# Performance work log

Measured on AMD Instinct MI355X. Metric: run time of the kernel, lower is better.

The kernel has to match this reference:

```python
import jax, jax.numpy as jnp
import numpy as np

NUM_HEADS = 12
LOCAL_WINDOW = 7


def setup_inputs() -> dict:
    key = jax.random.key(0)
    k1, k2, k3 = jax.random.split(key, 3)
    B, N, C = 2, 2048, 768
    x = jax.random.normal(k1, (B, N, C), dtype=jnp.float32)
    w_qkv = jax.random.normal(k2, (3 * C, C), dtype=jnp.float32) * (C ** -0.5)
    w_proj = jax.random.normal(k3, (C, C), dtype=jnp.float32) * (C ** -0.5)
    b_proj = jnp.zeros((C,), dtype=jnp.float32)
    return {"x": x, "w_qkv": w_qkv, "w_proj": w_proj, "b_proj": b_proj}


def reference(x, w_qkv, w_proj, b_proj):
    B, N, C = x.shape
    H = NUM_HEADS
    Dh = C // H
    scale = Dh ** -0.5
    # local-window additive mask: 0 within |i-j|<=w, -inf outside (vectorized)
    idx = jnp.arange(N)
    local_mask = jnp.where(
        jnp.abs(idx[:, None] - idx[None, :]) <= LOCAL_WINDOW, 0.0, -jnp.inf
    ).astype(x.dtype)
    qkv = x @ w_qkv.T
    qkv = qkv.reshape(B, N, 3, H, Dh).transpose(2, 0, 3, 1, 4)
    q, k, v = qkv[0], qkv[1], qkv[2]
    attn = jnp.einsum("bhnd,bhmd->bhnm", q, k) * scale
    attn = attn + local_mask[None, None, :, :]
    attn = jax.nn.softmax(attn, axis=-1)
    out = jnp.einsum("bhnm,bhmd->bhnd", attn, v)
    out = out.transpose(0, 2, 1, 3).reshape(B, N, C)
    return out @ w_proj.T + b_proj
```

## Files before the change

kernel.cpp:

```cpp
#include <hip/hip_runtime.h>
#include <hip/hip_bf16.h>

typedef __bf16 bf16;
typedef bf16 bf16x4 __attribute__((ext_vector_type(4)));
typedef bf16 bf16x8 __attribute__((ext_vector_type(8)));
typedef float floatx4 __attribute__((ext_vector_type(4)));

#define GLOBAL_AS __attribute__((address_space(1)))
#define LDS_AS __attribute__((address_space(3)))

__global__ __launch_bounds__(256)
void cvt3_f32_bf16(const float* __restrict__ s0, const float* __restrict__ s1,
                   const float* __restrict__ s2, bf16* __restrict__ d0,
                   bf16* __restrict__ d1, bf16* __restrict__ d2,
                   int n0, int n1, int n2)
{
    int t = blockIdx.x * blockDim.x + threadIdx.x;
    const float* s; bf16* d; int i;
    if (t < n0)                { s = s0; d = d0; i = t; }
    else if (t < n0 + n1)      { s = s1; d = d1; i = t - n0; }
    else if (t < n0 + n1 + n2) { s = s2; d = d2; i = t - n0 - n1; }
    else return;
    float4 v = ((const float4*)s)[i];
    bf16x4 o = { (bf16)v.x, (bf16)v.y, (bf16)v.z, (bf16)v.w };
    ((bf16x4*)d)[i] = o;
}

template<typename CT, bool AF32, bool WF32, int TM, int M, int N, int K,
         int LDA, int LDC>
__global__ __launch_bounds__(256, 2)
void gemm_bt(const void* __restrict__ Av, const void* __restrict__ Wv,
             CT* __restrict__ C, const float* __restrict__ bias)
{
    constexpr int MI = TM / 32;
    __shared__ __align__(16) bf16 As[TM * 32];
    __shared__ __align__(16) bf16 Bs[128 * 32];

    const int tid  = threadIdx.x;
    const int lane = tid & 63;
    const int wave = tid >> 6;
    const int row0 = blockIdx.x * TM;
    const int col0 = blockIdx.y * 128;

    const int wm = (wave & 1) * (TM / 2);
    const int wn = (wave >> 1) * 64;

    floatx4 acc[MI][4] = {};

    const int fr = lane & 15;
    const int fk = (lane >> 4) * 8;

    const int lr = lane >> 2;
    const int lk = (lane & 3) * 8;

    for (int k0 = 0; k0 < K; k0 += 32) {
        if (AF32) {
            constexpr int NV = TM * 4;
            #pragma unroll
            for (int c = 0; c < NV / 256; ++c) {
                const int idx = tid + c * 256;
                const int r   = idx >> 2;
                const int cb  = (idx & 3) * 8;
                const float4* g = (const float4*)((const float*)Av
                                   + (size_t)(row0 + r) * LDA + k0 + cb);
                float4 g0 = g[0], g1 = g[1];
                bf16x8 va;
                va[0]=(bf16)g0.x; va[1]=(bf16)g0.y; va[2]=(bf16)g0.z; va[3]=(bf16)g0.w;
                va[4]=(bf16)g1.x; va[5]=(bf16)g1.y; va[6]=(bf16)g1.z; va[7]=(bf16)g1.w;
                *(bf16x8*)(As + r * 32 + cb) = va;
            }
        } else {
            constexpr int CAW = TM / 64;
            #pragma unroll
            for (int c = 0; c < CAW; ++c) {
                const int chunk = wave * CAW + c;
                const int r = chunk * 16 + lr;
                const bf16* gA = (const bf16*)Av + (size_t)(row0 + r) * LDA + k0 + lk;
                __builtin_amdgcn_global_load_lds((const GLOBAL_AS void*)gA,
                                                 (LDS_AS void*)(As + chunk * 512),
                                                 16, 0, 0);
            }
        }
        if (WF32) {
            #pragma unroll
            for (int c = 0; c < 2; ++c) {
                const int idx = tid + c * 256;
                const int r   = idx >> 2;
                const int cb  = (idx & 3) * 8;
                const float4* g = (const float4*)((const float*)Wv
                                   + (size_t)(col0 + r) * K + k0 + cb);
                float4 g0 = g[0], g1 = g[1];
                bf16x8 vw;
                vw[0]=(bf16)g0.x; vw[1]=(bf16)g0.y; vw[2]=(bf16)g0.z; vw[3]=(bf16)g0.w;
                vw[4]=(bf16)g1.x; vw[5]=(bf16)g1.y; vw[6]=(bf16)g1.z; vw[7]=(bf16)g1.w;
                *(bf16x8*)(Bs + r * 32 + cb) = vw;
            }
        } else {
            #pragma unroll
            for (int c = 0; c < 2; ++c) {
                const int chunk = wave * 2 + c;
                const int r = chunk * 16 + lr;
                const bf16* gB = (const bf16*)Wv + (size_t)(col0 + r) * K + k0 + lk;
                __builtin_amdgcn_global_load_lds((const GLOBAL_AS void*)gB,
                                                 (LDS_AS void*)(Bs + chunk * 512),
                                                 16, 0, 0);
            }
        }
        __syncthreads();

        bf16x8 af[MI], bfr[4];
        #pragma unroll
        for (int i = 0; i < MI; ++i)
            af[i]  = *(const bf16x8*)(As + (wm + i * 16 + fr) * 32 + fk);
        #pragma unroll
        for (int j = 0; j < 4; ++j)
            bfr[j] = *(const bf16x8*)(Bs + (wn + j * 16 + fr) * 32 + fk);
        #pragma unroll
        for (int i = 0; i < MI; ++i)
            #pragma unroll
            for (int j = 0; j < 4; ++j)
                acc[i][j] = __builtin_amdgcn_mfma_f32_16x16x32_bf16(
                    af[i], bfr[j], acc[i][j], 0, 0, 0);

        __syncthreads();
    }

    const int fc  = lane & 15;
    const int fr4 = (lane >> 4) * 4;
    #pragma unroll
    for (int i = 0; i < MI; ++i) {
        #pragma unroll
        for (int j = 0; j < 4; ++j) {
            const int col = col0 + wn + j * 16 + fc;
            const float b = bias ? bias[col] : 0.0f;
            #pragma unroll
            for (int r = 0; r < 4; ++r) {
                const int row = row0 + wm + i * 16 + fr4 + r;
                C[(size_t)row * LDC + col] = (CT)(acc[i][j][r] + b);
            }
        }
    }
}

__global__ __launch_bounds__(256)
void attn_tile(const bf16* __restrict__ qkv, bf16* __restrict__ aout)
{
    __shared__ __align__(16) bf16 Ks[4][32][72];
    __shared__ __align__(16) bf16 Vt[4][64][40];
    __shared__ __align__(16) bf16 Ps[4][16][40];

    const int w    = threadIdx.x >> 6;
    const int lane = threadIdx.x & 63;
    const int c    = lane & 15;
    const int q    = lane >> 4;
    const int wid  = blockIdx.x * 4 + w;
    const int it   = wid & 127;
    const int bh   = wid >> 7;
    const int h    = bh % 12;
    const int b    = bh / 12;
    const int I0   = it * 16;
    const int bbase = b * 2048;
    const int j0   = I0 - 7;

    #pragma unroll
    for (int itr = 0; itr < 4; ++itr) {
        int idx = itr * 64 + lane;
        int row = idx >> 3;
        int dc  = (idx & 7) * 8;
        int jc  = j0 + row; jc = jc < 0 ? 0 : (jc > 2047 ? 2047 : jc);
        const bf16* base = qkv + (size_t)(bbase + jc) * 2304 + h * 64 + dc;
        bf16x8 kv = *(const bf16x8*)(base + 768);
        bf16x8 vv = *(const bf16x8*)(base + 1536);
        *(bf16x8*)(&Ks[w][row][dc]) = kv;
        #pragma unroll
        for (int e = 0; e < 8; ++e) Vt[w][dc + e][row] = vv[e];
    }

    const bf16* qrow = qkv + (size_t)(bbase + I0 + c) * 2304 + h * 64;
    bf16x8 aq0 = *(const bf16x8*)(qrow + q * 8);
    bf16x8 aq1 = *(const bf16x8*)(qrow + 32 + q * 8);

    __syncthreads();

    floatx4 st[2] = {};
    #pragma unroll
    for (int t = 0; t < 2; ++t) {
        bf16x8 k0 = *(const bf16x8*)(&Ks[w][t * 16 + c][q * 8]);
        bf16x8 k1 = *(const bf16x8*)(&Ks[w][t * 16 + c][32 + q * 8]);
        st[t] = __builtin_amdgcn_mfma_f32_16x16x32_bf16(aq0, k0, st[t], 0, 0, 0);
        st[t] = __builtin_amdgcn_mfma_f32_16x16x32_bf16(aq1, k1, st[t], 0, 0, 0);
    }

    float s[2][4];
    #pragma unroll
    for (int t = 0; t < 2; ++t)
        #pragma unroll
        for (int r = 0; r < 4; ++r) {
            int il = q * 4 + r;
            int jl = t * 16 + c;
            int ja = j0 + jl;
            bool valid = (jl >= il) && (jl <= il + 14) && (ja >= 0) && (ja < 2048);
            s[t][r] = valid ? st[t][r] * 0.125f : -1e30f;
        }

    float l[4], p[2][4];
    #pragma unroll
    for (int r = 0; r < 4; ++r) {
        float m2 = fmaxf(s[0][r], s[1][r]);
        #pragma unroll
        for (int mk = 1; mk < 16; mk <<= 1) m2 = fmaxf(m2, __shfl_xor(m2, mk, 64));
        p[0][r] = __expf(s[0][r] - m2);
        p[1][r] = __expf(s[1][r] - m2);
        float l2 = p[0][r] + p[1][r];
        #pragma unroll
        for (int mk = 1; mk < 16; mk <<= 1) l2 += __shfl_xor(l2, mk, 64);
        l[r] = l2;
    }

    #pragma unroll
    for (int r = 0; r < 4; ++r) {
        Ps[w][q * 4 + r][c]      = (bf16)p[0][r];
        Ps[w][q * 4 + r][16 + c] = (bf16)p[1][r];
    }
    __syncthreads();

    bf16x8 ap = *(const bf16x8*)(&Ps[w][c][q * 8]);
    floatx4 ov[4];
    #pragma unroll
    for (int nt = 0; nt < 4; ++nt) {
        bf16x8 vf = *(const bf16x8*)(&Vt[w][nt * 16 + c][q * 8]);
        floatx4 z = {};
        ov[nt] = __builtin_amdgcn_mfma_f32_16x16x32_bf16(ap, vf, z, 0, 0, 0);
    }

    float rl[4];
    #pragma unroll
    for (int r = 0; r < 4; ++r) rl[r] = 1.0f / l[r];
    #pragma unroll
    for (int r = 0; r < 4; ++r) {
        bf16* orow = aout + (size_t)(bbase + I0 + q * 4 + r) * 768 + h * 64;
        #pragma unroll
        for (int nt = 0; nt < 4; ++nt)
            orow[nt * 16 + c] = (bf16)(ov[nt][r] * rl[r]);
    }
}

extern "C" void kernel_launch(void* const* d_in, const int* in_sizes, int n_in,
                              void* d_out, int out_size, void* d_ws, size_t ws_size,
                              hipStream_t stream)
{
    const float* x      = (const float*)d_in[0];
    const float* w_qkv  = (const float*)d_in[1];
    const float* w_proj = (const float*)d_in[2];
    const float* b_proj = (const float*)d_in[3];
    float* out = (float*)d_out;

    bf16* qkv = (bf16*)d_ws;
    const size_t QKV_B  = (size_t)4096 * 2304 * 2;
    const size_t AO_B   = (size_t)4096 * 768 * 2;
    const size_t XB_B   = (size_t)4096 * 768 * 2;
    const size_t WQKV_B = (size_t)2304 * 768 * 2;
    const size_t WPRJ_B = (size_t)768 * 768 * 2;

    if (ws_size >= QKV_B + AO_B + XB_B + WQKV_B + WPRJ_B) {
        bf16* aout = (bf16*)((char*)d_ws + QKV_B);
        bf16* xb   = (bf16*)((char*)aout + AO_B);
        bf16* wqb  = (bf16*)((char*)xb + XB_B);
        bf16* wpb  = (bf16*)((char*)wqb + WQKV_B);

        const int n0 = 4096 * 768 / 4, n1 = 2304 * 768 / 4, n2 = 768 * 768 / 4;
        cvt3_f32_bf16<<<dim3((n0 + n1 + n2) / 256), 256, 0, stream>>>(
            x, w_qkv, w_proj, xb, wqb, wpb, n0, n1, n2);

        gemm_bt<bf16, false, false, 128, 4096, 2304, 768, 768, 2304>
            <<<dim3(32, 18), 256, 0, stream>>>(xb, wqb, qkv, nullptr);

        attn_tile<<<dim3(768), 256, 0, stream>>>(qkv, aout);

        gemm_bt<float, false, false, 64, 4096, 768, 768, 768, 768>
            <<<dim3(64, 6), 256, 0, stream>>>(aout, wpb, out, b_proj);
    } else {
        gemm_bt<bf16, true, true, 128, 4096, 2304, 768, 768, 2304>
            <<<dim3(32, 18), 256, 0, stream>>>(x, w_qkv, qkv, nullptr);

        bf16* aout = (bf16*)((char*)d_ws + QKV_B);
        attn_tile<<<dim3(768), 256, 0, stream>>>(qkv, aout);

        gemm_bt<float, false, true, 64, 4096, 768, 768, 768, 768>
            <<<dim3(64, 6), 256, 0, stream>>>(aout, w_proj, out, b_proj);
    }
}
```

Baseline: 123.4 us.

## Remap GEMM and attention blocks across XCDs, load K directly, swizzle V LDS

The GEMM block index is remapped so that consecutive row tiles land on the same XCD, and the attention block index is permuted the same way, both aimed at better L2 locality. In attention, K fragments now come straight from global memory into registers instead of being staged through LDS. The V transpose uses an XOR-swizzled LDS layout to reduce bank conflicts. Both __syncthreads calls are removed because each wave uses only its own LDS slice. That relies on wave-level ordering of LDS accesses, which is a correctness risk if the compiler or hardware reorders the writes and reads.

```diff
diff --git a/kernel.cpp b/kernel.cpp
--- a/kernel.cpp
+++ b/kernel.cpp
@@ -39,8 +39,16 @@
     const int tid  = threadIdx.x;
     const int lane = tid & 63;
     const int wave = tid >> 6;
-    const int row0 = blockIdx.x * TM;
-    const int col0 = blockIdx.y * 128;
+
+    const int lin = blockIdx.y * gridDim.x + blockIdx.x;
+    const int ch  = gridDim.x >> 3;
+    const int xcd = lin & 7;
+    const int rr  = lin >> 3;
+    const int bx  = xcd * ch + (rr % ch);
+    const int by  = rr / ch;
+
+    const int row0 = bx * TM;
+    const int col0 = by * 128;
 
     const int wm = (wave & 1) * (TM / 2);
     const int wn = (wave >> 1) * 64;
@@ -145,7 +153,6 @@
 __global__ __launch_bounds__(256)
 void attn_tile(const bf16* __restrict__ qkv, bf16* __restrict__ aout)
 {
-    __shared__ __align__(16) bf16 Ks[4][32][72];
     __shared__ __align__(16) bf16 Vt[4][64][40];
     __shared__ __align__(16) bf16 Ps[4][16][40];
 
@@ -153,7 +160,9 @@
     const int lane = threadIdx.x & 63;
     const int c    = lane & 15;
     const int q    = lane >> 4;
-    const int wid  = blockIdx.x * 4 + w;
+    int bid = blockIdx.x;
+    bid = (bid & 7) * 96 + (bid >> 3);
+    const int wid  = bid * 4 + w;
     const int it   = wid & 127;
     const int bh   = wid >> 7;
     const int h    = bh % 12;
@@ -168,25 +177,28 @@
         int row = idx >> 3;
         int dc  = (idx & 7) * 8;
         int jc  = j0 + row; jc = jc < 0 ? 0 : (jc > 2047 ? 2047 : jc);
-        const bf16* base = qkv + (size_t)(bbase + jc) * 2304 + h * 64 + dc;
-        bf16x8 kv = *(const bf16x8*)(base + 768);
-        bf16x8 vv = *(const bf16x8*)(base + 1536);
-        *(bf16x8*)(&Ks[w][row][dc]) = kv;
-        #pragma unroll
-        for (int e = 0; e < 8; ++e) Vt[w][dc + e][row] = vv[e];
+        const bf16* base = qkv + (size_t)(bbase + jc) * 2304 + 1536 + h * 64 + dc;
+        bf16x8 vv = *(const bf16x8*)base;
+        #pragma unroll
+        for (int e = 0; e < 8; ++e) {
+            int d    = dc + e;
+            int col2 = (row * 2) ^ (((d >> 3) & 3) << 4);
+            *(bf16*)((char*)&Vt[w][d][0] + col2) = vv[e];
+        }
     }
 
     const bf16* qrow = qkv + (size_t)(bbase + I0 + c) * 2304 + h * 64;
     bf16x8 aq0 = *(const bf16x8*)(qrow + q * 8);
     bf16x8 aq1 = *(const bf16x8*)(qrow + 32 + q * 8);
 
-    __syncthreads();
-
     floatx4 st[2] = {};
     #pragma unroll
     for (int t = 0; t < 2; ++t) {
-        bf16x8 k0 = *(const bf16x8*)(&Ks[w][t * 16 + c][q * 8]);
-        bf16x8 k1 = *(const bf16x8*)(&Ks[w][t * 16 + c][32 + q * 8]);
+        int jr = j0 + t * 16 + c;
+        jr = jr < 0 ? 0 : (jr > 2047 ? 2047 : jr);
+        const bf16* krow = qkv + (size_t)(bbase + jr) * 2304 + 768 + h * 64;
+        bf16x8 k0 = *(const bf16x8*)(krow + q * 8);
+        bf16x8 k1 = *(const bf16x8*)(krow + 32 + q * 8);
         st[t] = __builtin_amdgcn_mfma_f32_16x16x32_bf16(aq0, k0, st[t], 0, 0, 0);
         st[t] = __builtin_amdgcn_mfma_f32_16x16x32_bf16(aq1, k1, st[t], 0, 0, 0);
     }
@@ -222,13 +234,14 @@
         Ps[w][q * 4 + r][c]      = (bf16)p[0][r];
         Ps[w][q * 4 + r][16 + c] = (bf16)p[1][r];
     }
-    __syncthreads();
 
     bf16x8 ap = *(const bf16x8*)(&Ps[w][c][q * 8]);
     floatx4 ov[4];
     #pragma unroll
     for (int nt = 0; nt < 4; ++nt) {
-        bf16x8 vf = *(const bf16x8*)(&Vt[w][nt * 16 + c][q * 8]);
+        int dr = nt * 16 + c;
+        int cb = (q * 16) ^ (((dr >> 3) & 3) << 4);
+        bf16x8 vf = *(const bf16x8*)((const char*)&Vt[w][dr][0] + cb);
         floatx4 z = {};
         ov[nt] = __builtin_amdgcn_mfma_f32_16x16x32_bf16(ap, vf, z, 0, 0, 0);
     }
```

Result: no change. 121.9 us (-1.2%).
